# Kernel tuning notes

Measured on AMD Instinct MI355X. Metric: run time of the kernel, lower is better.

The kernel has to match this reference:

```python
import jax, jax.numpy as jnp
import numpy as np

B, T, H, NEX, ED = 65536, 20, 10, 13, 3

def _p(k, shape):
    return (jax.random.normal(k, shape, jnp.float32) * 0.1)

def setup_inputs() -> dict:
    key = jax.random.key(0)
    ks = jax.random.split(key, 24)
    e = jax.random.randint(ks[0], (B, T), 0, NEX, dtype=jnp.int32)
    f = jax.random.normal(ks[1], (B, T, 3), jnp.float32)
    emb = _p(ks[2], (NEX, ED)).at[0].set(0.0)  # row 0 zeroed as in torch init
    feat_w = _p(ks[3], (3, 3))
    feat_b = _p(ks[4], (3,))
    d = {"e": e, "f": f, "emb": emb, "feat_w": feat_w, "feat_b": feat_b}
    i = 5
    for layer, insz in ((0, 6), (1, 2 * H)):
        for sfx in ("", "r"):
            d[f"w_ih_l{layer}{sfx}"] = _p(ks[i], (4 * H, insz)); i += 1
            d[f"w_hh_l{layer}{sfx}"] = _p(ks[i], (4 * H, H)); i += 1
            d[f"b_ih_l{layer}{sfx}"] = _p(ks[i], (4 * H,)); i += 1
            d[f"b_hh_l{layer}{sfx}"] = _p(ks[i], (4 * H,)); i += 1
    return d

def _lstm_dir(x, w_ih, w_hh, b_ih, b_hh, reverse):
    # x: (B, T, I) -> hidden sequence (B, T, H). PyTorch gate order: i, f, g, o.
    xs = jnp.swapaxes(x, 0, 1)                      # (T, B, I)
    pre = xs @ w_ih.T + (b_ih + b_hh)               # input contribution, (T, B, 4H)
    def step(carry, p):
        h, c = carry
        g = p + h @ w_hh.T
        i, fg, gg, o = jnp.split(g, 4, axis=-1)
        c = jax.nn.sigmoid(fg) * c + jax.nn.sigmoid(i) * jnp.tanh(gg)
        h = jax.nn.sigmoid(o) * jnp.tanh(c)
        return (h, c), h
    nb = x.shape[0]
    init = (jnp.zeros((nb, H), x.dtype), jnp.zeros((nb, H), x.dtype))
    _, hs = jax.lax.scan(step, init, pre, reverse=reverse)
    return jnp.swapaxes(hs, 0, 1)                   # (B, T, H)

def _bilstm_layer(x, pf, pb):
    hf = _lstm_dir(x, *pf, reverse=False)
    hb = _lstm_dir(x, *pb, reverse=True)
    return jnp.concatenate([hf, hb], axis=-1)       # (B, T, 2H)

def reference(e, f, emb, feat_w, feat_b,
              w_ih_l0, w_hh_l0, b_ih_l0, b_hh_l0,
              w_ih_l0r, w_hh_l0r, b_ih_l0r, b_hh_l0r,
              w_ih_l1, w_hh_l1, b_ih_l1, b_hh_l1,
              w_ih_l1r, w_hh_l1r, b_ih_l1r, b_hh_l1r):
    ev = emb[e]                                     # (B, T, 3)
    f3 = f.reshape(-1, T, 3)
    mask = (f3[:, :, 1] != 0).astype(f.dtype)       # (B, T)
    fv = f3 @ feat_w.T + feat_b                     # (B, T, 3)
    x = jnp.concatenate([ev, fv], axis=2)           # (B, T, 6)
    x = _bilstm_layer(x, (w_ih_l0, w_hh_l0, b_ih_l0, b_hh_l0),
                         (w_ih_l0r, w_hh_l0r, b_ih_l0r, b_hh_l0r))
    x = _bilstm_layer(x, (w_ih_l1, w_hh_l1, b_ih_l1, b_hh_l1),
                         (w_ih_l1r, w_hh_l1r, b_ih_l1r, b_hh_l1r))
    ipe = jax.nn.relu(x[:, :, -1] * mask)           # last channel = backward dir unit H-1
    total = ipe.sum(axis=1, keepdims=True)          # (B, 1)
    return (total, ipe)
```

## Files before the change

### kernel.cpp

```cpp
#include <hip/hip_runtime.h>

#define BB 65536
#define TT 20
#define NBLK 2048

#define WS_WGT 0
#define WS_HF0 4096
#define PK1 0x00003C00u

#define LOG2E  1.442695041f
#define LOG2E2 2.885390082f

typedef unsigned u32;
typedef __fp16 f16x8 __attribute__((ext_vector_type(8)));
typedef float   f32x16 __attribute__((ext_vector_type(16)));
typedef u32     u32x4 __attribute__((ext_vector_type(4)));
typedef __fp16  h2v   __attribute__((ext_vector_type(2)));

__device__ __forceinline__ float sigmoid_f(float x) {
    float t = __builtin_amdgcn_exp2f(-LOG2E * x);
    return __builtin_amdgcn_rcpf(1.0f + t);
}
__device__ __forceinline__ float tanh_f(float x) {
    float t = __builtin_amdgcn_exp2f(LOG2E2 * x);
    return 1.0f - 2.0f * __builtin_amdgcn_rcpf(t + 1.0f);
}
__device__ __forceinline__ u32 pk_h16(float a, float b) {
    h2v v = __builtin_amdgcn_cvt_pkrtz(a, b);
    return __builtin_bit_cast(u32, v);
}
__device__ __forceinline__ f32x16 MFMA(u32x4 a, u32x4 b, f32x16 c) {
    return __builtin_amdgcn_mfma_f32_32x32x16_f16(
        __builtin_bit_cast(f16x8, a), __builtin_bit_cast(f16x8, b), c, 0, 0, 0);
}

__device__ __forceinline__ u32x4 pack_h(const float* h, bool hi, int xaddr, u32 b3) {
    u32 send = hi ? pk_h16(h[3], h[4]) : __float_as_uint(h[4]);
    u32 recv = (u32)__builtin_amdgcn_ds_bpermute(xaddr, (int)send);
    u32 lo0 = pk_h16(h[0], h[1]), lo1 = pk_h16(h[2], h[3]);
    u32 hi0 = pk_h16(__uint_as_float(recv), h[0]);
    u32 hi1 = pk_h16(h[1], h[2]);
    u32x4 b;
    b[0] = hi ? hi0 : lo0;
    b[1] = hi ? hi1 : lo1;
    b[2] = hi ? 0u : recv;
    b[3] = b3;
    return b;
}

__device__ __forceinline__ void cell_update5(const f32x16 a0, const f32x16 a1,
                                             float* c, float* h) {
#pragma unroll
    for (int v = 0; v < 4; ++v) {
        float cv = fmaf(sigmoid_f(a0[4 + v]), c[v], sigmoid_f(a0[v]) * tanh_f(a0[8 + v]));
        c[v] = cv;
        h[v] = sigmoid_f(a0[12 + v]) * tanh_f(cv);
    }
    float cv = fmaf(sigmoid_f(a1[1]), c[4], sigmoid_f(a1[0]) * tanh_f(a1[2]));
    c[4] = cv;
    h[4] = sigmoid_f(a1[3]) * tanh_f(cv);
}

__device__ __forceinline__ int inv_pi(int row) {
    if (row < 32) { int q = row >> 3, rem = row & 7; return q * 10 + 5 * (rem >> 2) + (rem & 3); }
    if (row < 40) { int lo = row - 32; return (lo & 3) * 10 + 5 * (lo >> 2) + 4; }
    return -1;
}

__global__ __launch_bounds__(256)
void prep_mfma(
    const float* __restrict__ wih0, const float* __restrict__ whh0,
    const float* __restrict__ bih0, const float* __restrict__ bhh0,
    const float* __restrict__ wih0r,const float* __restrict__ whh0r,
    const float* __restrict__ bih0r,const float* __restrict__ bhh0r,
    const float* __restrict__ wih1r,const float* __restrict__ whh1r,
    const float* __restrict__ bih1r,const float* __restrict__ bhh1r,
    u32* __restrict__ ws)
{
    for (int gid = threadIdx.x; gid < 14 * 64 * 4; gid += 256) {
        int fid = gid >> 8, l = (gid >> 2) & 63, j = gid & 3;
        int g = l >> 5;
        int tile, chunk;
        if (fid < 8) { tile = (fid >> 1) & 1; chunk = fid & 1; }
        else         { int q = fid - 8; tile = q / 3; chunk = q % 3; }
        int row = tile * 32 + (l & 31);
        int orow = inv_pi(row);
        int kb = (j >> 1) * 8 + 4 * g + (j & 1) * 2;
        float v[2] = {0.f, 0.f};
        if (orow >= 0) {
#pragma unroll
            for (int s = 0; s < 2; ++s) {
                int k = kb + s;
                float val = 0.f;
                if (fid < 8) {
                    bool bwd = fid >= 4;
                    if (chunk == 0) {
                        if (k < 6)       val = (bwd ? wih0r : wih0)[orow * 6 + k];
                        else if (k == 6) val = (bwd ? bih0r[orow] + bhh0r[orow]
                                                    : bih0[orow] + bhh0[orow]);
                    } else {
                        if (k < 10)      val = (bwd ? whh0r : whh0)[orow * 10 + k];
                    }
                } else {
                    if (chunk == 0)      { if (k < 10) val = wih1r[orow * 20 + k]; }
                    else if (chunk == 1) { if (k < 10) val = wih1r[orow * 20 + 10 + k]; }
                    else {
                        if (k < 10)      val = whh1r[orow * 10 + k];
                        else if (k == 10) val = bih1r[orow] + bhh1r[orow];
                    }
                }
                v[s] = val;
            }
        }
        ws[WS_WGT + (fid * 64 + l) * 4 + j] = pk_h16(v[0], v[1]);
    }
}

template<bool WS> struct Lds {
    u32   x[TT][3][32];
    float m[TT][32];
    u32   hf[WS ? 1 : TT][160];
};

template<bool WS>
__global__ __launch_bounds__(64)
void bilstm_mfma(
    const int*   __restrict__ eidx, const float* __restrict__ f,
    const float* __restrict__ emb,  const float* __restrict__ fw,
    const float* __restrict__ fb,
    const u32* __restrict__ wsr, u32* __restrict__ ghf,
    float* __restrict__ out)
{
    __shared__ Lds<WS> lds;
    const int  lane = threadIdx.x;
    const int  e    = lane & 31;
    const bool hi   = lane >= 32;
    const int  wid  = blockIdx.x;
    const int  b0   = wid * 32;
    const int  xaddr = (lane ^ 32) << 2;
    u32* hfp = ghf + (size_t)wid * TT * 160;

    {
        float fw0=fw[0],fw1=fw[1],fw2=fw[2],fw3=fw[3],fw4=fw[4];
        float fw5=fw[5],fw6=fw[6],fw7=fw[7],fw8=fw[8];
        float fb0=fb[0],fb1=fb[1],fb2=fb[2];
#pragma unroll 1
        for (int it = 0; it < 10; ++it) {
            int idx = lane + it * 64;
            int ee = idx / 20, t = idx - ee * 20;
            int gi = (b0 + ee) * TT + t;
            float f0 = f[gi * 3], f1 = f[gi * 3 + 1], f2v = f[gi * 3 + 2];
            int ei = eidx[gi] * 3;
            float x0 = emb[ei], x1 = emb[ei + 1], x2 = emb[ei + 2];
            float x3 = fmaf(fw0, f0, fmaf(fw1, f1, fmaf(fw2, f2v, fb0)));
            float x4 = fmaf(fw3, f0, fmaf(fw4, f1, fmaf(fw5, f2v, fb1)));
            float x5 = fmaf(fw6, f0, fmaf(fw7, f1, fmaf(fw8, f2v, fb2)));
            lds.x[t][0][ee] = pk_h16(x0, x1);
            lds.x[t][1][ee] = pk_h16(x2, x3);
            lds.x[t][2][ee] = pk_h16(x4, x5);
            lds.m[t][ee]    = (f1 != 0.f) ? 1.f : 0.f;
        }
    }

    const u32x4* wv = (const u32x4*)wsr;
    {
        u32x4 wf0 = wv[0 * 64 + lane], wf1 = wv[1 * 64 + lane];
        u32x4 wf2 = wv[2 * 64 + lane], wf3 = wv[3 * 64 + lane];
        float cf[5] = {0,0,0,0,0}, hv[5] = {0,0,0,0,0};
#pragma unroll 1
        for (int t = 0; t < TT; ++t) {
            u32 x01 = lds.x[t][0][e], x23 = lds.x[t][1][e], x45 = lds.x[t][2][e];
            u32x4 bx; bx[0] = hi ? x45 : x01; bx[1] = hi ? PK1 : x23; bx[2] = 0u; bx[3] = 0u;
            u32x4 bh = pack_h(hv, hi, xaddr, 0u);
            f32x16 z = {};
            f32x16 a0 = MFMA(wf0, bx, z); a0 = MFMA(wf1, bh, a0);
            f32x16 a1 = MFMA(wf2, bx, z); a1 = MFMA(wf3, bh, a1);
            cell_update5(a0, a1, cf, hv);
            u32x4 st = pack_h(hv, hi, xaddr, 0u);
            if (WS) {
                *(uint2*)(hfp + t * 160 + lane * 2) = make_uint2(st[0], st[1]);
                if (!hi) hfp[t * 160 + 128 + e] = st[2];
            } else {
                lds.hf[t][lane * 2] = st[0]; lds.hf[t][lane * 2 + 1] = st[1];
                if (!hi) lds.hf[t][128 + e] = st[2];
            }
        }
    }

    {
        u32x4 wb0 = wv[4 * 64 + lane], wb1 = wv[5 * 64 + lane];
        u32x4 wb2 = wv[6 * 64 + lane], wb3 = wv[7 * 64 + lane];
        u32x4 wB0 = wv[8 * 64 + lane], wB1 = wv[9 * 64 + lane], wB2 = wv[10 * 64 + lane];
        u32x4 wB3 = wv[11 * 64 + lane], wB4 = wv[12 * 64 + lane], wB5 = wv[13 * 64 + lane];
        float cb[5] = {0,0,0,0,0}, hbv[5] = {0,0,0,0,0};
        float cc[5] = {0,0,0,0,0}, h1v[5] = {0,0,0,0,0};
        float tot = 0.f;
#pragma unroll 1
        for (int t = TT - 1; t >= 0; --t) {
            uint2 ld2; u32 ldw;
            if (WS) { ld2 = *(const uint2*)(hfp + t * 160 + lane * 2);
                      ldw = hfp[t * 160 + 128 + e]; }
            else    { ld2 = make_uint2(lds.hf[t][lane * 2], lds.hf[t][lane * 2 + 1]);
                      ldw = lds.hf[t][128 + e]; }
            u32 x01 = lds.x[t][0][e], x23 = lds.x[t][1][e], x45 = lds.x[t][2][e];
            u32x4 bx; bx[0] = hi ? x45 : x01; bx[1] = hi ? PK1 : x23; bx[2] = 0u; bx[3] = 0u;
            u32x4 bh = pack_h(hbv, hi, xaddr, 0u);
            f32x16 z = {};
            f32x16 a0 = MFMA(wb0, bx, z); a0 = MFMA(wb1, bh, a0);
            f32x16 a1 = MFMA(wb2, bx, z); a1 = MFMA(wb3, bh, a1);
            cell_update5(a0, a1, cb, hbv);
            u32x4 bhf; bhf[0] = ld2.x; bhf[1] = ld2.y; bhf[2] = hi ? 0u : ldw; bhf[3] = 0u;
            u32x4 bhb = pack_h(hbv, hi, xaddr, 0u);
            u32x4 bh1 = pack_h(h1v, hi, xaddr, hi ? 0u : PK1);
            a0 = MFMA(wB0, bhf, z); a0 = MFMA(wB1, bhb, a0); a0 = MFMA(wB2, bh1, a0);
            a1 = MFMA(wB3, bhf, z); a1 = MFMA(wB4, bhb, a1); a1 = MFMA(wB5, bh1, a1);
            cell_update5(a0, a1, cc, h1v);
            if (hi) {
                float ip = fmaxf(h1v[4] * lds.m[t][e], 0.f);
                out[BB + (b0 + e) * TT + t] = ip;
                tot += ip;
            }
        }
        if (hi) out[b0 + e] = tot;
    }
}

extern "C" void kernel_launch(void* const* d_in, const int* in_sizes, int n_in,
                              void* d_out, int out_size, void* d_ws, size_t ws_size,
                              hipStream_t stream) {
    const int*   eidx  = (const int*)  d_in[0];
    const float* f     = (const float*)d_in[1];
    const float* emb   = (const float*)d_in[2];
    const float* fw    = (const float*)d_in[3];
    const float* fb    = (const float*)d_in[4];
    const float* wih0  = (const float*)d_in[5];
    const float* whh0  = (const float*)d_in[6];
    const float* bih0  = (const float*)d_in[7];
    const float* bhh0  = (const float*)d_in[8];
    const float* wih0r = (const float*)d_in[9];
    const float* whh0r = (const float*)d_in[10];
    const float* bih0r = (const float*)d_in[11];
    const float* bhh0r = (const float*)d_in[12];
    const float* wih1r = (const float*)d_in[17];
    const float* whh1r = (const float*)d_in[18];
    const float* bih1r = (const float*)d_in[19];
    const float* bhh1r = (const float*)d_in[20];
    float* out = (float*)d_out;
    u32* ws = (u32*)d_ws;

    hipLaunchKernelGGL(prep_mfma, dim3(1), dim3(256), 0, stream,
                       wih0, whh0, bih0, bhh0, wih0r, whh0r, bih0r, bhh0r,
                       wih1r, whh1r, bih1r, bhh1r, ws);

    const size_t need = (size_t)(WS_HF0 + (size_t)NBLK * TT * 160) * 4;
    dim3 grid(NBLK), block(64);
    if (ws_size >= need) {
        hipLaunchKernelGGL(bilstm_mfma<true>, grid, block, 0, stream,
                           eidx, f, emb, fw, fb, ws, ws + WS_HF0, out);
    } else {
        hipLaunchKernelGGL(bilstm_mfma<false>, grid, block, 0, stream,
                           eidx, f, emb, fw, fb, ws, ws + WS_HF0, out);
    }
}
```

Measured before the change: 72.85 us.

## Software-pipeline LSTM recurrences and fuse gate nonlinearities with shared reciprocals

```diff
diff --git a/kernel.cpp b/kernel.cpp
--- a/kernel.cpp
+++ b/kernel.cpp
@@ -17,14 +17,6 @@
 typedef u32     u32x4 __attribute__((ext_vector_type(4)));
 typedef __fp16  h2v   __attribute__((ext_vector_type(2)));
 
-__device__ __forceinline__ float sigmoid_f(float x) {
-    float t = __builtin_amdgcn_exp2f(-LOG2E * x);
-    return __builtin_amdgcn_rcpf(1.0f + t);
-}
-__device__ __forceinline__ float tanh_f(float x) {
-    float t = __builtin_amdgcn_exp2f(LOG2E2 * x);
-    return 1.0f - 2.0f * __builtin_amdgcn_rcpf(t + 1.0f);
-}
 __device__ __forceinline__ u32 pk_h16(float a, float b) {
     h2v v = __builtin_amdgcn_cvt_pkrtz(a, b);
     return __builtin_bit_cast(u32, v);
@@ -32,6 +24,20 @@
 __device__ __forceinline__ f32x16 MFMA(u32x4 a, u32x4 b, f32x16 c) {
     return __builtin_amdgcn_mfma_f32_32x32x16_f16(
         __builtin_bit_cast(f16x8, a), __builtin_bit_cast(f16x8, b), c, 0, 0, 0);
+}
+
+__device__ __forceinline__ void unit_cr(float ai, float af, float ag, float ao,
+                                        float* c, float* h) {
+    float pi = __builtin_amdgcn_exp2f(-LOG2E * ai);
+    float pf = __builtin_amdgcn_exp2f(-LOG2E * af);
+    float q  = __builtin_amdgcn_exp2f(LOG2E2 * ag);
+    float fv = __builtin_amdgcn_rcpf(1.0f + pf);
+    float ig = (q - 1.0f) * __builtin_amdgcn_rcpf((1.0f + pi) * (q + 1.0f));
+    float cv = fmaf(fv, *c, ig);
+    *c = cv;
+    float po = __builtin_amdgcn_exp2f(-LOG2E * ao);
+    float qc = __builtin_amdgcn_exp2f(LOG2E2 * cv);
+    *h = (qc - 1.0f) * __builtin_amdgcn_rcpf((1.0f + po) * (qc + 1.0f));
 }
 
 __device__ __forceinline__ u32x4 pack_h(const float* h, bool hi, int xaddr, u32 b3) {
@@ -51,14 +57,9 @@
 __device__ __forceinline__ void cell_update5(const f32x16 a0, const f32x16 a1,
                                              float* c, float* h) {
 #pragma unroll
-    for (int v = 0; v < 4; ++v) {
-        float cv = fmaf(sigmoid_f(a0[4 + v]), c[v], sigmoid_f(a0[v]) * tanh_f(a0[8 + v]));
-        c[v] = cv;
-        h[v] = sigmoid_f(a0[12 + v]) * tanh_f(cv);
-    }
-    float cv = fmaf(sigmoid_f(a1[1]), c[4], sigmoid_f(a1[0]) * tanh_f(a1[2]));
-    c[4] = cv;
-    h[4] = sigmoid_f(a1[3]) * tanh_f(cv);
+    for (int v = 0; v < 4; ++v)
+        unit_cr(a0[v], a0[4 + v], a0[8 + v], a0[12 + v], &c[v], &h[v]);
+    unit_cr(a1[0], a1[1], a1[2], a1[3], &c[4], &h[4]);
 }
 
 __device__ __forceinline__ int inv_pi(int row) {
@@ -163,18 +164,30 @@
     }
 
     const u32x4* wv = (const u32x4*)wsr;
+    const f32x16 zf = {};
+
     {
         u32x4 wf0 = wv[0 * 64 + lane], wf1 = wv[1 * 64 + lane];
         u32x4 wf2 = wv[2 * 64 + lane], wf3 = wv[3 * 64 + lane];
         float cf[5] = {0,0,0,0,0}, hv[5] = {0,0,0,0,0};
+        u32x4 bx0;
+        {
+            u32 x01 = lds.x[0][0][e], x23 = lds.x[0][1][e], x45 = lds.x[0][2][e];
+            bx0[0] = hi ? x45 : x01; bx0[1] = hi ? PK1 : x23; bx0[2] = 0u; bx0[3] = 0u;
+        }
+        f32x16 a0x = MFMA(wf0, bx0, zf);
+        f32x16 a1x = MFMA(wf2, bx0, zf);
 #pragma unroll 1
         for (int t = 0; t < TT; ++t) {
-            u32 x01 = lds.x[t][0][e], x23 = lds.x[t][1][e], x45 = lds.x[t][2][e];
-            u32x4 bx; bx[0] = hi ? x45 : x01; bx[1] = hi ? PK1 : x23; bx[2] = 0u; bx[3] = 0u;
             u32x4 bh = pack_h(hv, hi, xaddr, 0u);
-            f32x16 z = {};
-            f32x16 a0 = MFMA(wf0, bx, z); a0 = MFMA(wf1, bh, a0);
-            f32x16 a1 = MFMA(wf2, bx, z); a1 = MFMA(wf3, bh, a1);
+            f32x16 a0 = MFMA(wf1, bh, a0x);
+            f32x16 a1 = MFMA(wf3, bh, a1x);
+            if (t + 1 < TT) {
+                u32 x01 = lds.x[t+1][0][e], x23 = lds.x[t+1][1][e], x45 = lds.x[t+1][2][e];
+                u32x4 bx; bx[0] = hi ? x45 : x01; bx[1] = hi ? PK1 : x23; bx[2] = 0u; bx[3] = 0u;
+                a0x = MFMA(wf0, bx, zf);
+                a1x = MFMA(wf2, bx, zf);
+            }
             cell_update5(a0, a1, cf, hv);
             u32x4 st = pack_h(hv, hi, xaddr, 0u);
             if (WS) {
@@ -195,33 +208,59 @@
         float cb[5] = {0,0,0,0,0}, hbv[5] = {0,0,0,0,0};
         float cc[5] = {0,0,0,0,0}, h1v[5] = {0,0,0,0,0};
         float tot = 0.f;
+
+        {
+            u32 x01 = lds.x[TT-1][0][e], x23 = lds.x[TT-1][1][e], x45 = lds.x[TT-1][2][e];
+            u32x4 bx; bx[0] = hi ? x45 : x01; bx[1] = hi ? PK1 : x23; bx[2] = 0u; bx[3] = 0u;
+            f32x16 a0 = MFMA(wb0, bx, zf);
+            f32x16 a1 = MFMA(wb2, bx, zf);
+            cell_update5(a0, a1, cb, hbv);
+        }
+        uint2 cur2; u32 curw;
+        if (WS) { cur2 = *(const uint2*)(hfp + (TT-1) * 160 + lane * 2);
+                  curw = hfp[(TT-1) * 160 + 128 + e]; }
+        else    { cur2 = make_uint2(lds.hf[TT-1][lane * 2], lds.hf[TT-1][lane * 2 + 1]);
+                  curw = lds.hf[TT-1][128 + e]; }
+
 #pragma unroll 1
-        for (int t = TT - 1; t >= 0; --t) {
-            uint2 ld2; u32 ldw;
-            if (WS) { ld2 = *(const uint2*)(hfp + t * 160 + lane * 2);
-                      ldw = hfp[t * 160 + 128 + e]; }
-            else    { ld2 = make_uint2(lds.hf[t][lane * 2], lds.hf[t][lane * 2 + 1]);
-                      ldw = lds.hf[t][128 + e]; }
-            u32 x01 = lds.x[t][0][e], x23 = lds.x[t][1][e], x45 = lds.x[t][2][e];
+        for (int t = TT - 1; t >= 1; --t) {
+            uint2 nxt2; u32 nxtw;
+            if (WS) { nxt2 = *(const uint2*)(hfp + (t-1) * 160 + lane * 2);
+                      nxtw = hfp[(t-1) * 160 + 128 + e]; }
+            else    { nxt2 = make_uint2(lds.hf[t-1][lane * 2], lds.hf[t-1][lane * 2 + 1]);
+                      nxtw = lds.hf[t-1][128 + e]; }
+            u32x4 shared = pack_h(hbv, hi, xaddr, 0u);
+            u32x4 bh1    = pack_h(h1v, hi, xaddr, hi ? 0u : PK1);
+            u32x4 bhf; bhf[0] = cur2.x; bhf[1] = cur2.y; bhf[2] = hi ? 0u : curw; bhf[3] = 0u;
+            f32x16 B0 = MFMA(wB0, bhf, zf); B0 = MFMA(wB1, shared, B0); B0 = MFMA(wB2, bh1, B0);
+            f32x16 B1 = MFMA(wB3, bhf, zf); B1 = MFMA(wB4, shared, B1); B1 = MFMA(wB5, bh1, B1);
+            u32 x01 = lds.x[t-1][0][e], x23 = lds.x[t-1][1][e], x45 = lds.x[t-1][2][e];
             u32x4 bx; bx[0] = hi ? x45 : x01; bx[1] = hi ? PK1 : x23; bx[2] = 0u; bx[3] = 0u;
-            u32x4 bh = pack_h(hbv, hi, xaddr, 0u);
-            f32x16 z = {};
-            f32x16 a0 = MFMA(wb0, bx, z); a0 = MFMA(wb1, bh, a0);
-            f32x16 a1 = MFMA(wb2, bx, z); a1 = MFMA(wb3, bh, a1);
-            cell_update5(a0, a1, cb, hbv);
-            u32x4 bhf; bhf[0] = ld2.x; bhf[1] = ld2.y; bhf[2] = hi ? 0u : ldw; bhf[3] = 0u;
-            u32x4 bhb = pack_h(hbv, hi, xaddr, 0u);
-            u32x4 bh1 = pack_h(h1v, hi, xaddr, hi ? 0u : PK1);
-            a0 = MFMA(wB0, bhf, z); a0 = MFMA(wB1, bhb, a0); a0 = MFMA(wB2, bh1, a0);
-            a1 = MFMA(wB3, bhf, z); a1 = MFMA(wB4, bhb, a1); a1 = MFMA(wB5, bh1, a1);
-            cell_update5(a0, a1, cc, h1v);
+            f32x16 A0 = MFMA(wb0, bx, zf); A0 = MFMA(wb1, shared, A0);
+            f32x16 A1 = MFMA(wb2, bx, zf); A1 = MFMA(wb3, shared, A1);
+            cell_update5(B0, B1, cc, h1v);
             if (hi) {
                 float ip = fmaxf(h1v[4] * lds.m[t][e], 0.f);
                 out[BB + (b0 + e) * TT + t] = ip;
                 tot += ip;
             }
-        }
-        if (hi) out[b0 + e] = tot;
+            cell_update5(A0, A1, cb, hbv);
+            cur2 = nxt2; curw = nxtw;
+        }
+        {
+            u32x4 shared = pack_h(hbv, hi, xaddr, 0u);
+            u32x4 bh1    = pack_h(h1v, hi, xaddr, hi ? 0u : PK1);
+            u32x4 bhf; bhf[0] = cur2.x; bhf[1] = cur2.y; bhf[2] = hi ? 0u : curw; bhf[3] = 0u;
+            f32x16 B0 = MFMA(wB0, bhf, zf); B0 = MFMA(wB1, shared, B0); B0 = MFMA(wB2, bh1, B0);
+            f32x16 B1 = MFMA(wB3, bhf, zf); B1 = MFMA(wB4, shared, B1); B1 = MFMA(wB5, bh1, B1);
+            cell_update5(B0, B1, cc, h1v);
+            if (hi) {
+                float ip = fmaxf(h1v[4] * lds.m[0][e], 0.f);
+                out[BB + (b0 + e) * TT + 0] = ip;
+                tot += ip;
+                out[b0 + e] = tot;
+            }
+        }
     }
 }
 
```

Result: faster. 69.94 us (-4.0%).
